# Performance work log

Measured on AMD Instinct MI355X. Metric: run time of the kernel, lower is better.

Reference implementation:

```python
import jax, jax.numpy as jnp
import numpy as np

B, N, E = 128, 1024, 16384
ENTITY, EMB, HID = 100000, 100, 100


def setup_inputs() -> dict:
    key = jax.random.key(0)
    ks = jax.random.split(key, 13)
    s = 0.1  # param init scale
    return {
        "neighbors": jax.random.randint(ks[0], (B, N), 0, ENTITY),
        "adj_row": jax.random.randint(ks[1], (B, E), 0, N),
        "adj_col": jax.random.randint(ks[2], (B, E), 0, N),
        "adj_val": jax.random.uniform(ks[3], (B, E), jnp.float32),
        "emb_table": jax.random.normal(ks[4], (ENTITY, EMB), jnp.float32) * s,
        "gcn_w": jax.random.normal(ks[5], (EMB, HID), jnp.float32) * s,
        "gcn_b": jax.random.normal(ks[6], (HID,), jnp.float32) * s,
        "w_ih": jax.random.normal(ks[7], (3 * HID, HID), jnp.float32) * s,
        "w_hh": jax.random.normal(ks[8], (3 * HID, HID), jnp.float32) * s,
        "b_ih": jax.random.normal(ks[9], (3 * HID,), jnp.float32) * s,
        "b_hh": jax.random.normal(ks[10], (3 * HID,), jnp.float32) * s,
        "fc1_w": jax.random.normal(ks[11], (HID, HID), jnp.float32) * s,
        "fc1_b": jax.random.normal(ks[12], (HID,), jnp.float32) * s,
    }


def reference(neighbors, adj_row, adj_col, adj_val, emb_table,
              gcn_w, gcn_b, w_ih, w_hh, b_ih, b_hh, fc1_w, fc1_b):
    n_nodes = neighbors.shape[1]
    # Embedding lookup: [B, N, EMB]
    x = emb_table[neighbors]
    # GCN layer: support = X @ W, then sparse adj @ support, then + bias
    support = jnp.einsum('bne,eh->bnh', x, gcn_w)  # [B, N, HID]

    def spmm(row, col, val, sup):
        # out[r] += val * sup[col]  (per-sample sparse aggregation)
        return jax.ops.segment_sum(val[:, None] * sup[col], row,
                                   num_segments=n_nodes)

    seq = jax.vmap(spmm)(adj_row, adj_col, adj_val, support) + gcn_b  # [B,N,HID]

    # GRU over node sequence (PyTorch gate order: r, z, n)
    def gru_step(h, x_t):
        gx = x_t @ w_ih.T + b_ih
        gh = h @ w_hh.T + b_hh
        xr, xz, xn = jnp.split(gx, 3, axis=-1)
        hr, hz, hn = jnp.split(gh, 3, axis=-1)
        r = jax.nn.sigmoid(xr + hr)
        z = jax.nn.sigmoid(xz + hz)
        n = jnp.tanh(xn + r * hn)
        h_new = (1.0 - z) * n + z * h
        return h_new, None

    h0 = jnp.zeros((seq.shape[0], w_hh.shape[1]), seq.dtype)
    h, _ = jax.lax.scan(gru_step, h0, seq.transpose(1, 0, 2))  # final hidden [B,HID]

    # h.permute(1,0,2) -> [B, 1, HID], then relu(fc1(.))
    return jax.nn.relu(h[:, None, :] @ fc1_w.T + fc1_b)
```

## Files before the change

kernel.cpp:

```cpp
#include <hip/hip_runtime.h>
#include <hip/hip_bf16.h>


typedef unsigned int u32;
typedef float f2 __attribute__((ext_vector_type(2)));

__device__ __forceinline__ float bflo(u32 u) {
    union { u32 i; float f; } v; v.i = u << 16; return v.f;
}
__device__ __forceinline__ float bfhi(u32 u) {
    union { u32 i; float f; } v; v.i = u & 0xffff0000u; return v.f;
}
__device__ __forceinline__ u32 f2bf1(float f) {
    union { float f; u32 u; } v; v.f = f;
    return (v.u + 0x7fffu + ((v.u >> 16) & 1u)) >> 16;
}
__device__ __forceinline__ u32 packbf(float a, float b) {
    return f2bf1(a) | (f2bf1(b) << 16);
}
__device__ __forceinline__ float sigm(float x) { return 1.f / (1.f + __expf(-x)); }
__device__ __forceinline__ float tanh_fast(float x) {
    float e = __expf(2.f * x);
    return 1.f - 2.f / (e + 1.f);
}

__global__ __launch_bounds__(256, 2)
void gcn_kernel(const int* __restrict__ nb, const float* __restrict__ emb,
                const float* __restrict__ w, u32* __restrict__ support)
{
    __shared__ float wl[10000];
    for (int i = threadIdx.x; i < 10000; i += 256) wl[i] = w[i];
    __syncthreads();

    const int n = blockIdx.x * 256 + threadIdx.x;
    const long long row = nb[n];
    const float4* __restrict__ xr = (const float4*)(emb + row * 100);

    float acc[100];
#pragma unroll
    for (int h = 0; h < 100; ++h) acc[h] = 0.f;

    for (int kk = 0; kk < 25; ++kk) {
        const float4 xv = xr[kk];
        const float xs[4] = { xv.x, xv.y, xv.z, xv.w };
#pragma unroll
        for (int q = 0; q < 4; ++q) {
            const float* wrow = &wl[(kk * 4 + q) * 100];
            const float xq = xs[q];
#pragma unroll
            for (int h4 = 0; h4 < 25; ++h4) {
                const float4 w4 = *(const float4*)(wrow + h4 * 4);
                acc[h4*4+0] = fmaf(xq, w4.x, acc[h4*4+0]);
                acc[h4*4+1] = fmaf(xq, w4.y, acc[h4*4+1]);
                acc[h4*4+2] = fmaf(xq, w4.z, acc[h4*4+2]);
                acc[h4*4+3] = fmaf(xq, w4.w, acc[h4*4+3]);
            }
        }
    }

    u32* __restrict__ o = support + (size_t)n * 50;
#pragma unroll
    for (int i = 0; i < 50; ++i) o[i] = packbf(acc[2*i], acc[2*i+1]);
}

__global__ __launch_bounds__(256, 2)
void csr_build(const int* __restrict__ arow, const int* __restrict__ acol,
               const float* __restrict__ aval,
               int* __restrict__ offs, int2* __restrict__ csr)
{
    __shared__ int cnt[1024];
    __shared__ int part[256];
    __shared__ int offl[1024];

    const int b   = blockIdx.x;
    const int tid = threadIdx.x;
    const int*   rw = arow + b * 16384;
    const int*   cl = acol + b * 16384;
    const float* vl = aval + b * 16384;

    for (int i = tid; i < 1024; i += 256) cnt[i] = 0;
    __syncthreads();
    for (int e = tid; e < 16384; e += 256) atomicAdd(&cnt[rw[e]], 1);
    __syncthreads();

    int c[4]; int s = 0;
#pragma unroll
    for (int q = 0; q < 4; ++q) { c[q] = cnt[tid * 4 + q]; s += c[q]; }
    part[tid] = s;
    __syncthreads();
    for (int off = 1; off < 256; off <<= 1) {
        int v = (tid >= off) ? part[tid - off] : 0;
        __syncthreads();
        part[tid] += v;
        __syncthreads();
    }
    int run = part[tid] - s;
#pragma unroll
    for (int q = 0; q < 4; ++q) { offl[tid * 4 + q] = run; run += c[q]; }
    __syncthreads();

    for (int i = tid; i < 1024; i += 256) offs[b * 1025 + i] = offl[i];
    if (tid == 0) offs[b * 1025 + 1024] = 16384;

    int2* cs = csr + (size_t)b * 16384;
    for (int e = tid; e < 16384; e += 256) {
        const int r   = rw[e];
        const int pos = atomicAdd(&offl[r], 1);
        int2 cv; cv.x = cl[e]; cv.y = __float_as_int(vl[e]);
        cs[pos] = cv;
    }
}

__global__ __launch_bounds__(256, 4)
void spmm_agg(const int* __restrict__ offs, const int2* __restrict__ csr,
              const u32* __restrict__ support,
              const float* __restrict__ gcn_b, u32* __restrict__ seq)
{
    const int b    = blockIdx.y;
    const int lr   = threadIdx.x / 50;
    const int lane = threadIdx.x % 50;
    const int r    = blockIdx.x * 5 + lr;
    if (lr >= 5 || r >= 1024) return;

    const int e0 = offs[b * 1025 + r];
    const int e1 = offs[b * 1025 + r + 1];
    const int2* __restrict__ cs = csr + (size_t)b * 16384;
    const u32* __restrict__ supb = support + (size_t)b * 1024 * 50;

    float a0 = 0.f, a1 = 0.f;
    for (int e = e0; e < e1; ++e) {
        const int2 cv = cs[e];
        const float v = __int_as_float(cv.y);
        const u32 u = supb[(size_t)cv.x * 50 + lane];
        a0 = fmaf(v, bflo(u), a0);
        a1 = fmaf(v, bfhi(u), a1);
    }
    a0 += gcn_b[2 * lane];
    a1 += gcn_b[2 * lane + 1];
    seq[((size_t)b * 1024 + r) * 50 + lane] = packbf(a0, a1);
}

__global__ __launch_bounds__(256, 2)
void gx_gemm0(const u32* __restrict__ seq, const float* __restrict__ w_ih,
              const float* __restrict__ b_ih, u32* __restrict__ gxW,
              int c0, int ctl, int CT)
{
    __shared__ float wl[10000];
    const int g    = blockIdx.x % 3;
    const int tile = blockIdx.x / 3;
    const int tid  = threadIdx.x;

    for (int i = tid; i < 10000; i += 256)
        wl[(i % 100) * 100 + (i / 100)] = w_ih[g * 10000 + i];
    __syncthreads();

    const int m = tile * 256 + tid;
    const int b = m >> ctl;
    const int t = m & (CT - 1);
    const uint2* sr2 = (const uint2*)(seq + ((size_t)b * 1024 + c0 + t) * 50);

    float acc[100];
    const float4* bi4 = (const float4*)(b_ih + g * 100);
#pragma unroll
    for (int j4 = 0; j4 < 25; ++j4) {
        const float4 bv = bi4[j4];
        acc[j4*4+0] = bv.x; acc[j4*4+1] = bv.y; acc[j4*4+2] = bv.z; acc[j4*4+3] = bv.w;
    }

    for (int kk = 0; kk < 25; ++kk) {
        const uint2 up = sr2[kk];
        const float xs[4] = { bflo(up.x), bfhi(up.x), bflo(up.y), bfhi(up.y) };
#pragma unroll
        for (int q = 0; q < 4; ++q) {
            const float* wrow = &wl[(kk * 4 + q) * 100];
            const float xq = xs[q];
#pragma unroll
            for (int j4 = 0; j4 < 25; ++j4) {
                const float4 w4 = *(const float4*)(wrow + j4 * 4);
                acc[j4*4+0] = fmaf(xq, w4.x, acc[j4*4+0]);
                acc[j4*4+1] = fmaf(xq, w4.y, acc[j4*4+1]);
                acc[j4*4+2] = fmaf(xq, w4.z, acc[j4*4+2]);
                acc[j4*4+3] = fmaf(xq, w4.w, acc[j4*4+3]);
            }
        }
    }

    u32* og = gxW + (size_t)m * 150 + g * 50;
#pragma unroll
    for (int i = 0; i < 50; ++i) og[i] = packbf(acc[2*i], acc[2*i+1]);
}

__global__ __launch_bounds__(256, 1)
void gru_v5(const u32* __restrict__ gxR, size_t sampStride,
            const float* __restrict__ w_hh, const float* __restrict__ b_hh,
            float* __restrict__ hg, const float* __restrict__ fc1_w,
            const float* __restrict__ fc1_b, float* __restrict__ out,
            int first, int last, int CT)
{
    __shared__ float hb[2][104];

    const int tid  = threadIdx.x;
    const int samp = blockIdx.x;
    const int j    = tid >> 1;
    const int p    = tid & 1;
    const int hi   = j & 1;
    const int jc   = (j < 100) ? j : 99;

    f2 wr[26], wz[26], wn[26];
    {
        const float* r0 = w_hh + (size_t)jc * 100;
#pragma unroll
        for (int i = 0; i < 13; ++i) {
            const int   q  = 2 * i + p;
            const int   qc = (q < 25) ? q : 24;
            const float m  = (q < 25) ? 1.f : 0.f;
            float4 v;
            v = *(const float4*)(r0 + 4 * qc);
            wr[2*i] = (f2){v.x * m, v.y * m}; wr[2*i+1] = (f2){v.z * m, v.w * m};
            v = *(const float4*)(r0 + 10000 + 4 * qc);
            wz[2*i] = (f2){v.x * m, v.y * m}; wz[2*i+1] = (f2){v.z * m, v.w * m};
            v = *(const float4*)(r0 + 20000 + 4 * qc);
            wn[2*i] = (f2){v.x * m, v.y * m}; wn[2*i+1] = (f2){v.z * m, v.w * m};
        }
    }

    const float bhr = b_hh[jc];
    const float bhz = b_hh[100 + jc];
    const float bhn = b_hh[200 + jc];
    float hreg = first ? 0.f : hg[samp * 100 + jc];

    if (tid < 200 && p == 0) hb[0][j] = hreg;
    if (tid >= 100 && tid < 104) { hb[0][tid] = 0.f; hb[1][tid] = 0.f; }
    __syncthreads();

    const int w50 = ((tid >> 2) < 50) ? (tid >> 2) : 49;
    const u32* gp = gxR + (size_t)samp * sampStride + w50;
    u32 a0 = gp[0],   a1 = gp[50],  a2 = gp[100];
    u32 b0 = gp[150], b1 = gp[200], b2 = gp[250];

    int cur = 0;

#define GRU_STEP(T, X0, X1, X2)                                               \
    {                                                                         \
        const float* hc = &hb[cur][4 * p];                                    \
        f2 ar0 = {0.f,0.f}, ar1 = {0.f,0.f};                                  \
        f2 az0 = {0.f,0.f}, az1 = {0.f,0.f};                                  \
        f2 an0 = {0.f,0.f}, an1 = {0.f,0.f};                                  \
        _Pragma("unroll")                                                     \
        for (int i = 0; i < 13; ++i) {                                        \
            const float4 hv = *(const float4*)(hc + 8 * i);                   \
            const f2 h01 = {hv.x, hv.y}, h23 = {hv.z, hv.w};                  \
            ar0 += wr[2*i]   * h01;  ar1 += wr[2*i+1] * h23;                  \
            az0 += wz[2*i]   * h01;  az1 += wz[2*i+1] * h23;                  \
            an0 += wn[2*i]   * h01;  an1 += wn[2*i+1] * h23;                  \
        }                                                                     \
        const u32 c0 = X0, c1 = X1, c2 = X2;                                  \
        if ((T) + 2 < CT) {                                                   \
            const u32* q2 = gp + (size_t)((T) + 2) * 150;                     \
            X0 = q2[0]; X1 = q2[50]; X2 = q2[100];                            \
        }                                                                     \
        float sr = (ar0.x + ar0.y) + (ar1.x + ar1.y);                         \
        float sz = (az0.x + az0.y) + (az1.x + az1.y);                         \
        float sn = (an0.x + an0.y) + (an1.x + an1.y);                         \
        sr += __shfl_xor(sr, 1);                                              \
        sz += __shfl_xor(sz, 1);                                              \
        sn += __shfl_xor(sn, 1);                                              \
        const float gxr = hi ? bfhi(c0) : bflo(c0);                           \
        const float gxz = hi ? bfhi(c1) : bflo(c1);                           \
        const float gxn = hi ? bfhi(c2) : bflo(c2);                           \
        const float rg  = sigm(gxr + sr + bhr);                               \
        const float zg  = sigm(gxz + sz + bhz);                               \
        const float ng  = tanh_fast(gxn + rg * (sn + bhn));                   \
        hreg = (1.f - zg) * ng + zg * hreg;                                   \
        if (tid < 200 && p == 0) hb[cur ^ 1][j] = hreg;                       \
        __syncthreads();                                                      \
        cur ^= 1;                                                             \
    }

    for (int t = 0; t < CT; t += 2) {
        GRU_STEP(t,     a0, a1, a2);
        GRU_STEP(t + 1, b0, b1, b2);
    }
#undef GRU_STEP

    if (tid < 200 && p == 0) hg[samp * 100 + j] = hreg;
    if (last && tid < 100) {
        const float* hc = hb[cur];
        const float4* fw = (const float4*)(fc1_w + (size_t)tid * 100);
        float s0 = 0.f, s1 = 0.f, s2 = 0.f, s3 = 0.f;
#pragma unroll
        for (int kk = 0; kk < 25; ++kk) {
            const float4 wv = fw[kk];
            const float4 hv = *(const float4*)(hc + kk * 4);
            s0 = fmaf(wv.x, hv.x, s0);
            s1 = fmaf(wv.y, hv.y, s1);
            s2 = fmaf(wv.z, hv.z, s2);
            s3 = fmaf(wv.w, hv.w, s3);
        }
        const float s = (s0 + s1) + (s2 + s3) + fc1_b[tid];
        out[samp * 100 + tid] = fmaxf(s, 0.f);
    }
}

extern "C" void kernel_launch(void* const* d_in, const int* in_sizes, int n_in,
                              void* d_out, int out_size, void* d_ws, size_t ws_size,
                              hipStream_t stream)
{
    const int*   neighbors = (const int*)  d_in[0];
    const int*   adj_row   = (const int*)  d_in[1];
    const int*   adj_col   = (const int*)  d_in[2];
    const float* adj_val   = (const float*)d_in[3];
    const float* emb       = (const float*)d_in[4];
    const float* gcn_w     = (const float*)d_in[5];
    const float* gcn_b     = (const float*)d_in[6];
    const float* w_ih      = (const float*)d_in[7];
    const float* w_hh      = (const float*)d_in[8];
    const float* b_ih      = (const float*)d_in[9];
    const float* b_hh      = (const float*)d_in[10];
    const float* fc1_w     = (const float*)d_in[11];
    const float* fc1_b     = (const float*)d_in[12];
    float* out = (float*)d_out;

    char* ws = (char*)d_ws;
    const size_t seq_bytes     = (size_t)128 * 1024 * 50 * 4;
    const size_t hg_bytes      = 128 * 100 * 4;
    const size_t support_bytes = (size_t)128 * 1024 * 50 * 4;
    const size_t offs_bytes    = (size_t)128 * 1025 * 4;

    u32*   seq = (u32*)ws;
    float* hg  = (float*)(ws + seq_bytes);
    char*  rest = ws + seq_bytes + hg_bytes;
    const size_t rest_avail = ws_size - seq_bytes - hg_bytes;

    u32*  support = (u32*)rest;
    int*  offs    = (int*)(rest + support_bytes);
    int2* csr     = (int2*)(rest + support_bytes + offs_bytes);

    gcn_kernel<<<512, 256, 0, stream>>>(neighbors, emb, gcn_w, support);
    csr_build<<<128, 256, 0, stream>>>(adj_row, adj_col, adj_val, offs, csr);
    spmm_agg<<<dim3(205, 128), 256, 0, stream>>>(offs, csr, support, gcn_b, seq);

    const size_t gx_full = (size_t)128 * 1024 * 150 * 4;
    u32* gx = (u32*)rest;

    if (rest_avail >= gx_full) {
        gx_gemm0<<<1536, 256, 0, stream>>>(seq, w_ih, b_ih, gx, 0, 10, 1024);
        gru_v5<<<128, 256, 0, stream>>>(gx, (size_t)1024 * 150, w_hh, b_hh, hg,
                                        fc1_w, fc1_b, out, 1, 1, 1024);
    } else {
        int CT = 512, ctl = 9;
        while (CT > 8 && (size_t)128 * CT * 150 * 4 > rest_avail) { CT >>= 1; --ctl; }
        const int nch = 1024 / CT;
        for (int c = 0; c < nch; ++c) {
            gx_gemm0<<<3 * (128 * CT / 256), 256, 0, stream>>>(seq, w_ih, b_ih, gx,
                                                               c * CT, ctl, CT);
            gru_v5<<<128, 256, 0, stream>>>(gx, (size_t)CT * 150, w_hh, b_hh, hg,
                                            fc1_w, fc1_b, out,
                                            (c == 0) ? 1 : 0, (c == nch - 1) ? 1 : 0, CT);
        }
    }
}
```

Before: 1.173 ms.

## Store GRU hidden state and recurrent weights as bf16 and use dot2 instructions

The GRU recurrence kernel now keeps w_hh in registers as packed bf16 pairs and broadcasts the hidden state through shared memory as packed bf16. The per-step matvec uses v_dot2_f32_bf16, roughly halving FMA count and LDS read bytes. Shuffle-based pair reductions and hidden-state packing use DPP moves instead. This targets the latency of the serial 1024-step recurrence, but rounding h to bf16 each step can accumulate error.

New measurement: 1.185 ms. No clear change (+1.0%).

```diff
diff --git a/kernel.cpp b/kernel.cpp
--- a/kernel.cpp
+++ b/kernel.cpp
@@ -191,13 +191,13 @@
 }
 
 __global__ __launch_bounds__(256, 1)
-void gru_v5(const u32* __restrict__ gxR, size_t sampStride,
-            const float* __restrict__ w_hh, const float* __restrict__ b_hh,
-            float* __restrict__ hg, const float* __restrict__ fc1_w,
-            const float* __restrict__ fc1_b, float* __restrict__ out,
-            int first, int last, int CT)
-{
-    __shared__ float hb[2][104];
+void gru_v13(const u32* __restrict__ gxR, size_t sampStride,
+             const float* __restrict__ w_hh, const float* __restrict__ b_hh,
+             float* __restrict__ hg, const float* __restrict__ fc1_w,
+             const float* __restrict__ fc1_b, float* __restrict__ out,
+             int first, int last, int CT)
+{
+    __shared__ u32 hb[2][64];
 
     const int tid  = threadIdx.x;
     const int samp = blockIdx.x;
@@ -206,22 +206,33 @@
     const int hi   = j & 1;
     const int jc   = (j < 100) ? j : 99;
 
-    f2 wr[26], wz[26], wn[26];
+#define WDECL(g) u32 g##_0,g##_1,g##_2,g##_3,g##_4,g##_5,g##_6,g##_7,g##_8,   \
+    g##_9,g##_10,g##_11,g##_12,g##_13,g##_14,g##_15,g##_16,g##_17,g##_18,     \
+    g##_19,g##_20,g##_21,g##_22,g##_23,g##_24,g##_25,g##_26,g##_27
+    WDECL(wr); WDECL(wz); WDECL(wn);
+#undef WDECL
     {
-        const float* r0 = w_hh + (size_t)jc * 100;
-#pragma unroll
-        for (int i = 0; i < 13; ++i) {
-            const int   q  = 2 * i + p;
-            const int   qc = (q < 25) ? q : 24;
-            const float m  = (q < 25) ? 1.f : 0.f;
-            float4 v;
-            v = *(const float4*)(r0 + 4 * qc);
-            wr[2*i] = (f2){v.x * m, v.y * m}; wr[2*i+1] = (f2){v.z * m, v.w * m};
-            v = *(const float4*)(r0 + 10000 + 4 * qc);
-            wz[2*i] = (f2){v.x * m, v.y * m}; wz[2*i+1] = (f2){v.z * m, v.w * m};
-            v = *(const float4*)(r0 + 20000 + 4 * qc);
-            wn[2*i] = (f2){v.x * m, v.y * m}; wn[2*i+1] = (f2){v.z * m, v.w * m};
-        }
+        const float* rr = w_hh + (size_t)jc * 100;
+        const float* rz = rr + 10000;
+        const float* rn = rr + 20000;
+#define WSLOT(s)                                                              \
+        {                                                                     \
+            const int  m    = 24 * p + (s);                                   \
+            const int  real = p ? ((s) >= 1 && (s) <= 25) : ((s) <= 24);      \
+            const int  mc   = (m < 50) ? m : 49;                              \
+            float2 wv;                                                        \
+            wv = *(const float2*)(rr + 2 * mc);                               \
+            wr_##s = real ? packbf(wv.x, wv.y) : 0u;                          \
+            wv = *(const float2*)(rz + 2 * mc);                               \
+            wz_##s = real ? packbf(wv.x, wv.y) : 0u;                          \
+            wv = *(const float2*)(rn + 2 * mc);                               \
+            wn_##s = real ? packbf(wv.x, wv.y) : 0u;                          \
+        }
+        WSLOT(0)  WSLOT(1)  WSLOT(2)  WSLOT(3)  WSLOT(4)  WSLOT(5)  WSLOT(6)
+        WSLOT(7)  WSLOT(8)  WSLOT(9)  WSLOT(10) WSLOT(11) WSLOT(12) WSLOT(13)
+        WSLOT(14) WSLOT(15) WSLOT(16) WSLOT(17) WSLOT(18) WSLOT(19) WSLOT(20)
+        WSLOT(21) WSLOT(22) WSLOT(23) WSLOT(24) WSLOT(25) WSLOT(26) WSLOT(27)
+#undef WSLOT
     }
 
     const float bhr = b_hh[jc];
@@ -229,8 +240,12 @@
     const float bhn = b_hh[200 + jc];
     float hreg = first ? 0.f : hg[samp * 100 + jc];
 
-    if (tid < 200 && p == 0) hb[0][j] = hreg;
-    if (tid >= 100 && tid < 104) { hb[0][tid] = 0.f; hb[1][tid] = 0.f; }
+    {
+        u32 hb16 = f2bf1(hreg);
+        u32 o16  = (u32)__builtin_amdgcn_mov_dpp((int)hb16, 0x4E, 0xF, 0xF, true);
+        if (tid < 200 && (tid & 3) == 0) hb[0][tid >> 2] = hb16 | (o16 << 16);
+    }
+    if (tid >= 100 && tid < 114) { hb[0][tid - 50] = 0u; hb[1][tid - 50] = 0u; }
     __syncthreads();
 
     const int w50 = ((tid >> 2) < 50) ? (tid >> 2) : 49;
@@ -240,31 +255,36 @@
 
     int cur = 0;
 
+#define DPPADD(s, CTRL)                                                       \
+    (s) += __int_as_float(__builtin_amdgcn_mov_dpp(                           \
+               __float_as_int(s), (CTRL), 0xF, 0xF, true))
+
+#define D2(acc, w, h) asm("v_dot2_f32_bf16 %0, %1, %2, %0"                    \
+                          : "+v"(acc) : "v"(w), "v"(h))
+
+#define SG(i, s0, s1, s2, s3)                                                 \
+    {                                                                         \
+        const uint4 hv = hc[i];                                               \
+        D2(ar0, wr_##s0, hv.x); D2(az0, wz_##s0, hv.x); D2(an0, wn_##s0, hv.x);\
+        D2(ar1, wr_##s1, hv.y); D2(az1, wz_##s1, hv.y); D2(an1, wn_##s1, hv.y);\
+        D2(ar0, wr_##s2, hv.z); D2(az0, wz_##s2, hv.z); D2(an0, wn_##s2, hv.z);\
+        D2(ar1, wr_##s3, hv.w); D2(az1, wz_##s3, hv.w); D2(an1, wn_##s3, hv.w);\
+    }
+
 #define GRU_STEP(T, X0, X1, X2)                                               \
     {                                                                         \
-        const float* hc = &hb[cur][4 * p];                                    \
-        f2 ar0 = {0.f,0.f}, ar1 = {0.f,0.f};                                  \
-        f2 az0 = {0.f,0.f}, az1 = {0.f,0.f};                                  \
-        f2 an0 = {0.f,0.f}, an1 = {0.f,0.f};                                  \
-        _Pragma("unroll")                                                     \
-        for (int i = 0; i < 13; ++i) {                                        \
-            const float4 hv = *(const float4*)(hc + 8 * i);                   \
-            const f2 h01 = {hv.x, hv.y}, h23 = {hv.z, hv.w};                  \
-            ar0 += wr[2*i]   * h01;  ar1 += wr[2*i+1] * h23;                  \
-            az0 += wz[2*i]   * h01;  az1 += wz[2*i+1] * h23;                  \
-            an0 += wn[2*i]   * h01;  an1 += wn[2*i+1] * h23;                  \
-        }                                                                     \
+        const uint4* hc = (const uint4*)(&hb[cur][24 * p]);                   \
+        float ar0 = 0.f, ar1 = 0.f, az0 = 0.f, az1 = 0.f, an0 = 0.f, an1 = 0.f;\
+        SG(0, 0, 1, 2, 3)   SG(1, 4, 5, 6, 7)   SG(2, 8, 9, 10, 11)           \
+        SG(3, 12, 13, 14, 15) SG(4, 16, 17, 18, 19) SG(5, 20, 21, 22, 23)     \
+        SG(6, 24, 25, 26, 27)                                                 \
         const u32 c0 = X0, c1 = X1, c2 = X2;                                  \
         if ((T) + 2 < CT) {                                                   \
             const u32* q2 = gp + (size_t)((T) + 2) * 150;                     \
             X0 = q2[0]; X1 = q2[50]; X2 = q2[100];                            \
         }                                                                     \
-        float sr = (ar0.x + ar0.y) + (ar1.x + ar1.y);                         \
-        float sz = (az0.x + az0.y) + (az1.x + az1.y);                         \
-        float sn = (an0.x + an0.y) + (an1.x + an1.y);                         \
-        sr += __shfl_xor(sr, 1);                                              \
-        sz += __shfl_xor(sz, 1);                                              \
-        sn += __shfl_xor(sn, 1);                                              \
+        float sr = ar0 + ar1, sz = az0 + az1, sn = an0 + an1;                 \
+        DPPADD(sr, 0xB1);  DPPADD(sz, 0xB1);  DPPADD(sn, 0xB1);               \
         const float gxr = hi ? bfhi(c0) : bflo(c0);                           \
         const float gxz = hi ? bfhi(c1) : bflo(c1);                           \
         const float gxn = hi ? bfhi(c2) : bflo(c2);                           \
@@ -272,7 +292,11 @@
         const float zg  = sigm(gxz + sz + bhz);                               \
         const float ng  = tanh_fast(gxn + rg * (sn + bhn));                   \
         hreg = (1.f - zg) * ng + zg * hreg;                                   \
-        if (tid < 200 && p == 0) hb[cur ^ 1][j] = hreg;                       \
+        u32 hb16 = f2bf1(hreg);                                               \
+        u32 o16  = (u32)__builtin_amdgcn_mov_dpp((int)hb16, 0x4E, 0xF, 0xF,   \
+                                                 true);                       \
+        if (tid < 200 && (tid & 3) == 0)                                      \
+            hb[cur ^ 1][tid >> 2] = hb16 | (o16 << 16);                       \
         __syncthreads();                                                      \
         cur ^= 1;                                                             \
     }
@@ -282,23 +306,32 @@
         GRU_STEP(t + 1, b0, b1, b2);
     }
 #undef GRU_STEP
+#undef SG
+#undef D2
+#undef DPPADD
 
     if (tid < 200 && p == 0) hg[samp * 100 + j] = hreg;
-    if (last && tid < 100) {
-        const float* hc = hb[cur];
-        const float4* fw = (const float4*)(fc1_w + (size_t)tid * 100);
-        float s0 = 0.f, s1 = 0.f, s2 = 0.f, s3 = 0.f;
-#pragma unroll
-        for (int kk = 0; kk < 25; ++kk) {
-            const float4 wv = fw[kk];
-            const float4 hv = *(const float4*)(hc + kk * 4);
-            s0 = fmaf(wv.x, hv.x, s0);
-            s1 = fmaf(wv.y, hv.y, s1);
-            s2 = fmaf(wv.z, hv.z, s2);
-            s3 = fmaf(wv.w, hv.w, s3);
-        }
-        const float s = (s0 + s1) + (s2 + s3) + fc1_b[tid];
-        out[samp * 100 + tid] = fmaxf(s, 0.f);
+
+    if (last) {
+        float* hf = (float*)hb;
+        __syncthreads();
+        if (tid < 200 && p == 0) hf[j] = hreg;
+        __syncthreads();
+        if (tid < 100) {
+            const float4* fw = (const float4*)(fc1_w + (size_t)tid * 100);
+            float s0 = 0.f, s1 = 0.f, s2 = 0.f, s3 = 0.f;
+#pragma unroll
+            for (int kk = 0; kk < 25; ++kk) {
+                const float4 wv = fw[kk];
+                const float4 hv = *(const float4*)(hf + kk * 4);
+                s0 = fmaf(wv.x, hv.x, s0);
+                s1 = fmaf(wv.y, hv.y, s1);
+                s2 = fmaf(wv.z, hv.z, s2);
+                s3 = fmaf(wv.w, hv.w, s3);
+            }
+            const float s = (s0 + s1) + (s2 + s3) + fc1_b[tid];
+            out[samp * 100 + tid] = fmaxf(s, 0.f);
+        }
     }
 }
 
@@ -345,8 +378,8 @@
 
     if (rest_avail >= gx_full) {
         gx_gemm0<<<1536, 256, 0, stream>>>(seq, w_ih, b_ih, gx, 0, 10, 1024);
-        gru_v5<<<128, 256, 0, stream>>>(gx, (size_t)1024 * 150, w_hh, b_hh, hg,
-                                        fc1_w, fc1_b, out, 1, 1, 1024);
+        gru_v13<<<128, 256, 0, stream>>>(gx, (size_t)1024 * 150, w_hh, b_hh, hg,
+                                         fc1_w, fc1_b, out, 1, 1, 1024);
     } else {
         int CT = 512, ctl = 9;
         while (CT > 8 && (size_t)128 * CT * 150 * 4 > rest_avail) { CT >>= 1; --ctl; }
@@ -354,9 +387,9 @@
         for (int c = 0; c < nch; ++c) {
             gx_gemm0<<<3 * (128 * CT / 256), 256, 0, stream>>>(seq, w_ih, b_ih, gx,
                                                                c * CT, ctl, CT);
-            gru_v5<<<128, 256, 0, stream>>>(gx, (size_t)CT * 150, w_hh, b_hh, hg,
-                                            fc1_w, fc1_b, out,
-                                            (c == 0) ? 1 : 0, (c == nch - 1) ? 1 : 0, CT);
-        }
-    }
-}
+            gru_v13<<<128, 256, 0, stream>>>(gx, (size_t)CT * 150, w_hh, b_hh, hg,
+                                             fc1_w, fc1_b, out,
+                                             (c == 0) ? 1 : 0, (c == nch - 1) ? 1 : 0, CT);
+        }
+    }
+}
```
